# Kernel optimization log

Measured on AMD Instinct MI355X. Metric: run time of the kernel, lower is better.

Reference implementation:

```python
import jax, jax.numpy as jnp
import numpy as np

DEPTH, DIM, HEADS, DIM_HEAD, NBF, MULT = 2, 512, 8, 64, 256, 4
INNER = HEADS * DIM_HEAD


def layernorm(x, g, b, eps=1e-5):
    mu = jnp.mean(x, axis=-1, keepdims=True)
    var = jnp.mean((x - mu) ** 2, axis=-1, keepdims=True)
    return (x - mu) * jax.lax.rsqrt(var + eps) * g + b


def softmax_kernel(data, proj, is_query, eps=1e-4):
    # data: [b,h,n,d], proj: [m,d]  -> phi: [b,h,n,m]  (FAVOR+ positive features)
    d = data.shape[-1]
    normalizer = d ** -0.25
    ratio = proj.shape[0] ** -0.5
    data_dash = jnp.einsum('bhnd,md->bhnm', data * normalizer, proj)
    diag = jnp.sum(data ** 2, axis=-1, keepdims=True) * 0.5 * (normalizer ** 2)
    if is_query:
        m = jnp.max(data_dash, axis=-1, keepdims=True)
    else:
        m = jnp.max(data_dash, axis=(-2, -1), keepdims=True)
    m = jax.lax.stop_gradient(m)
    return ratio * (jnp.exp(data_dash - diag - m) + eps)


def setup_inputs() -> dict:
    key = jax.random.key(0)
    ks = jax.random.split(key, 16)
    s = 0.02
    B, N = 4, 8192
    inp = {
        'x': jax.random.normal(ks[0], (B, N, DIM), jnp.float32),
        'ln1_g': jnp.ones((DEPTH, DIM), jnp.float32),
        'ln1_b': jnp.zeros((DEPTH, DIM), jnp.float32),
        'ln2_g': jnp.ones((DEPTH, DIM), jnp.float32),
        'ln2_b': jnp.zeros((DEPTH, DIM), jnp.float32),
        'Wq': jax.random.normal(ks[1], (DEPTH, DIM, INNER), jnp.float32) * s,
        'bq': jnp.zeros((DEPTH, INNER), jnp.float32),
        'Wk': jax.random.normal(ks[2], (DEPTH, DIM, INNER), jnp.float32) * s,
        'bk': jnp.zeros((DEPTH, INNER), jnp.float32),
        'Wv': jax.random.normal(ks[3], (DEPTH, DIM, INNER), jnp.float32) * s,
        'bv': jnp.zeros((DEPTH, INNER), jnp.float32),
        'Wo': jax.random.normal(ks[4], (DEPTH, INNER, DIM), jnp.float32) * s,
        'bo': jnp.zeros((DEPTH, DIM), jnp.float32),
        'proj': jax.random.normal(ks[5], (DEPTH, NBF, DIM_HEAD), jnp.float32),
        'W1': jax.random.normal(ks[6], (DEPTH, DIM, DIM * MULT), jnp.float32) * s,
        'b1': jnp.zeros((DEPTH, DIM * MULT), jnp.float32),
        'W2': jax.random.normal(ks[7], (DEPTH, DIM * MULT, DIM), jnp.float32) * s,
        'b2': jnp.zeros((DEPTH, DIM), jnp.float32),
    }
    return inp


def reference(x, ln1_g, ln1_b, ln2_g, ln2_b, Wq, bq, Wk, bk, Wv, bv, Wo, bo, proj, W1, b1, W2, b2):
    B, N, D = x.shape
    for i in range(DEPTH):
        # --- PreLayerNorm + FAVOR+ self-attention, residual ---
        y = layernorm(x, ln1_g[i], ln1_b[i])
        q = (y @ Wq[i] + bq[i]).reshape(B, N, HEADS, DIM_HEAD).transpose(0, 2, 1, 3)
        k = (y @ Wk[i] + bk[i]).reshape(B, N, HEADS, DIM_HEAD).transpose(0, 2, 1, 3)
        v = (y @ Wv[i] + bv[i]).reshape(B, N, HEADS, DIM_HEAD).transpose(0, 2, 1, 3)
        qp = softmax_kernel(q, proj[i], True)   # [b,h,n,m]
        kp = softmax_kernel(k, proj[i], False)  # [b,h,n,m]
        # non-causal linear attention: O(n*m*d) instead of O(n^2)
        k_sum = kp.sum(axis=2)                               # [b,h,m]
        d_inv = 1.0 / jnp.einsum('bhnm,bhm->bhn', qp, k_sum)
        ctx = jnp.einsum('bhnm,bhnd->bhmd', kp, v)           # [b,h,m,d]
        o = jnp.einsum('bhmd,bhnm,bhn->bhnd', ctx, qp, d_inv)
        o = o.transpose(0, 2, 1, 3).reshape(B, N, INNER)
        x = x + o @ Wo[i] + bo[i]
        # --- PreLayerNorm + FeedForward (GELU), residual ---
        y = layernorm(x, ln2_g[i], ln2_b[i])
        h = jax.nn.gelu(y @ W1[i] + b1[i], approximate=False)
        x = x + h @ W2[i] + b2[i]
    return x
```

## Files before the change

kernel.cpp:

```cpp
#include <hip/hip_runtime.h>
#include <math.h>

#define DIMX 512
#define HEADS 8
#define DHEAD 64
#define NBFX 256
#define FFD 2048
#define NBX 4
#define SEQ 8192
#define TOK (NBX*SEQ)
#define NBH (NBX*HEADS)
#define VROWS 80
#define NCHUNK 16
#define BK 64

typedef unsigned short u16;
typedef __attribute__((ext_vector_type(8))) short short8;
typedef __attribute__((ext_vector_type(4))) float f32x4;

__device__ __forceinline__ float bf2f(u16 x){ return __uint_as_float(((unsigned)x)<<16); }
__device__ __forceinline__ u16 f2bf(float f){
  unsigned u=__float_as_uint(f);
  return (u16)((u + 0x7FFFu + ((u>>16)&1u))>>16);
}
__device__ __forceinline__ void gload16(const void* g, void* l){
  __builtin_amdgcn_global_load_lds((const __attribute__((address_space(1))) void*)g,
                                   (__attribute__((address_space(3))) void*)l, 16, 0, 0);
}
__device__ __forceinline__ float gelu_f(float v){
  float x=v*0.70710678118654752f;
  float ax=fabsf(x);
  float t=1.0f/(1.0f+0.3275911f*ax);
  float p=t*(0.254829592f+t*(-0.284496736f+t*(1.421413741f+t*(-1.453152027f+t*1.061405429f))));
  float erfv=1.0f-p*__expf(-ax*ax);
  erfv=(x<0.0f)? -erfv : erfv;
  return 0.5f*v*(1.0f+erfv);
}

#define FENCE asm volatile(""::: "memory")
#define BAR() do{ FENCE; __builtin_amdgcn_s_barrier(); FENCE; }while(0)

__global__ void copy_f32(const float4* __restrict__ s, float4* __restrict__ d, int n4){
  int i=blockIdx.x*blockDim.x+threadIdx.x;
  if(i<n4) d[i]=s[i];
}
__global__ void conv_proj(const float* __restrict__ p, u16* __restrict__ o, int n){
  int i=blockIdx.x*blockDim.x+threadIdx.x;
  if(i<n) o[i]=f2bf(p[i]*0.35355339059327373f);
}
__global__ void convT(const float* __restrict__ src, u16* __restrict__ dst, int K, int Ncol){
  __shared__ float t[32][33];
  int k0=blockIdx.y*32, n0=blockIdx.x*32;
  int tx=threadIdx.x, ty=threadIdx.y;
  for(int i=ty;i<32;i+=8) t[i][tx]=src[(size_t)(k0+i)*Ncol + n0+tx];
  __syncthreads();
  for(int i=ty;i<32;i+=8) dst[(size_t)(n0+i)*K + k0+tx]=f2bf(t[tx][i]);
}
__global__ void fill_vt(u16* __restrict__ vt){
  int i=blockIdx.x*blockDim.x+threadIdx.x;
  int n=i&(SEQ-1); int r=(i>>13)&15; int bh=i>>17;
  vt[((size_t)bh*VROWS + 64 + r)*SEQ + n] = (r==0)? (u16)0x3F80 : (u16)0;
}
__global__ void pack_bias(const float* __restrict__ bq, const float* __restrict__ bk,
                          const float* __restrict__ bv, float* __restrict__ o){
  int i=blockIdx.x*blockDim.x+threadIdx.x;
  int l=i/1536, c=i-l*1536;
  const float* s=(c<512)? bq : ((c<1024)? bk : bv);
  o[i]=s[l*512 + (c&511)];
}

__global__ __launch_bounds__(256) void ln_k(const float* __restrict__ x, const float* __restrict__ g,
                                            const float* __restrict__ b, u16* __restrict__ y){
  const int row=blockIdx.x*4 + (threadIdx.x>>6);
  const int ln=threadIdx.x&63;
  const float* xr=x+(size_t)row*DIMX;
  float4 v0=*(const float4*)&xr[ln*8];
  float4 v1=*(const float4*)&xr[ln*8+4];
  float v[8]={v0.x,v0.y,v0.z,v0.w,v1.x,v1.y,v1.z,v1.w};
  float s=0;
  #pragma unroll
  for(int e=0;e<8;e++) s+=v[e];
  #pragma unroll
  for(int m=1;m<64;m<<=1) s+=__shfl_xor(s,m);
  const float mean=s*(1.0f/DIMX);
  float s2=0;
  #pragma unroll
  for(int e=0;e<8;e++){ v[e]-=mean; s2+=v[e]*v[e]; }
  #pragma unroll
  for(int m=1;m<64;m<<=1) s2+=__shfl_xor(s2,m);
  const float rs=rsqrtf(s2*(1.0f/DIMX)+1e-5f);
  u16* yr=y+(size_t)row*DIMX+ln*8;
  u16 pk[8];
  #pragma unroll
  for(int e=0;e<8;e++) pk[e]=f2bf(v[e]*rs*g[ln*8+e]+b[ln*8+e]);
  uint4 pv;
  pv.x=(unsigned)pk[0]|((unsigned)pk[1]<<16); pv.y=(unsigned)pk[2]|((unsigned)pk[3]<<16);
  pv.z=(unsigned)pk[4]|((unsigned)pk[5]<<16); pv.w=(unsigned)pk[6]|((unsigned)pk[7]<<16);
  *(uint4*)yr=pv;
}

#define MFMA16(MH,BF,NH) do{                                                             \
  __builtin_amdgcn_s_setprio(1);                                                         \
  _Pragma("unroll") for(int kk_=0;kk_<2;kk_++)                                           \
    _Pragma("unroll") for(int i_=0;i_<4;i_++)                                            \
      _Pragma("unroll") for(int j_=0;j_<2;j_++)                                          \
        acc[MH][i_][NH][j_]=__builtin_amdgcn_mfma_f32_16x16x32_bf16(af[i_][kk_],BF[j_][kk_],acc[MH][i_][NH][j_],0,0,0); \
  __builtin_amdgcn_s_setprio(0);                                                         \
}while(0)

#define STG(T,HALF,ISB,BUF) do{ if((T)<nt){                                              \
  gload16(gp[ISB][HALF][0]+(size_t)(T)*BK, &lds[BUF][ISB][(HALF)*128 +    wv*8][0]);     \
  gload16(gp[ISB][HALF][1]+(size_t)(T)*BK, &lds[BUF][ISB][(HALF)*128 + 64+wv*8][0]); } }while(0)

#define LDA(BUF,MH) do{                                                                  \
  _Pragma("unroll") for(int i_=0;i_<4;i_++)                                              \
    _Pragma("unroll") for(int kk_=0;kk_<2;kk_++)                                         \
      af[i_][kk_]=*(const short8*)((const u16*)lds[BUF][0] + aoffs[MH][i_][kk_]); }while(0)

#define LDB(BF,BUF,NH) do{                                                               \
  _Pragma("unroll") for(int j_=0;j_<2;j_++)                                              \
    _Pragma("unroll") for(int kk_=0;kk_<2;kk_++)                                         \
      BF[j_][kk_]=*(const short8*)((const u16*)lds[BUF][1] + boffs[NH][j_][kk_]); }while(0)

#define TILE(T,BUF,OBUF) do{                                                             \
  LDB(bf0,BUF,0); LDA(BUF,0);                                                            \
  STG((T)+1,1,0,OBUF);                                                                   \
  BAR(); MFMA16(0,bf0,0); BAR();                                                         \
  LDB(bf1,BUF,1);                                                                        \
  STG((T)+1,1,1,OBUF);                                                                   \
  BAR(); MFMA16(0,bf1,1); BAR();                                                         \
  LDA(BUF,1);                                                                            \
  STG((T)+2,0,1,BUF);                                                                    \
  BAR(); MFMA16(1,bf0,0); BAR();                                                         \
  STG((T)+2,0,0,BUF);                                                                    \
  BAR(); MFMA16(1,bf1,1);                                                                \
  if((T)+2<nt) asm volatile("s_waitcnt vmcnt(4)":::"memory");                            \
  else         asm volatile("s_waitcnt vmcnt(0)":::"memory");                            \
  BAR();                                                                                 \
}while(0)

template<int EPI,int K>
__global__ __launch_bounds__(512,2) void gemm256(const u16* __restrict__ A, const u16* __restrict__ Bt,
                                                 const float* __restrict__ bias, void* __restrict__ outp,
                                                 u16* __restrict__ out2, int Ncol){
  constexpr int nt=K/BK;
  __shared__ u16 lds[2][2][256][64];
  const int tid=threadIdx.x, wv=tid>>6, ln=tid&63;
  const int wr=wv>>2, wc=wv&3;
  const int gx=gridDim.x, gy=gridDim.y;
  const int P=blockIdx.y*gx+blockIdx.x;
  const int band=gy>>3;
  const int xcd=P&7, sI=P>>3;
  const int by=xcd*band + (sI - (sI/band)*band);
  const int bx=sI/band;
  const int m0=by*256, n0=bx*256;
  f32x4 acc[2][4][2][2]={};

  const u16* gp[2][2][2];
  #pragma unroll
  for(int isB=0;isB<2;isB++)
    #pragma unroll
    for(int half=0;half<2;half++)
      #pragma unroll
      for(int s=0;s<2;s++){
        int G=s*512+wv*64+ln;
        int arow=half*128+(G>>3), g=G&7;
        const u16* src=isB? Bt:A;
        int b0=isB? n0:m0;
        gp[isB][half][s]=src+(size_t)(b0+arow)*K+((g^(arow&7))<<3);
      }
  int aoffs[2][4][2], boffs[2][2][2];
  #pragma unroll
  for(int mh=0;mh<2;mh++)
    #pragma unroll
    for(int i=0;i<4;i++){
      int row=wr*128+mh*64+i*16+(ln&15);
      #pragma unroll
      for(int kk=0;kk<2;kk++)
        aoffs[mh][i][kk]=row*64+((((kk*4+(ln>>4)))^(row&7))<<3);
    }
  #pragma unroll
  for(int nh=0;nh<2;nh++)
    #pragma unroll
    for(int j=0;j<2;j++){
      int row=wc*64+nh*32+j*16+(ln&15);
      #pragma unroll
      for(int kk=0;kk<2;kk++)
        boffs[nh][j][kk]=row*64+((((kk*4+(ln>>4)))^(row&7))<<3);
    }

  short8 af[4][2], bf0[2][2], bf1[2][2];

  STG(0,0,0,0); STG(0,1,0,0); STG(0,0,1,0); STG(0,1,1,0);
  STG(1,0,1,1); STG(1,0,0,1);
  asm volatile("s_waitcnt vmcnt(4)":::"memory");
  BAR();

  #pragma unroll 1
  for(int t=0;t<nt;t+=2){
    TILE(t,0,1);
    TILE(t+1,1,0);
  }

  #pragma unroll
  for(int mh=0;mh<2;mh++)
  #pragma unroll
  for(int i=0;i<4;i++)
  #pragma unroll
  for(int nh=0;nh<2;nh++)
  #pragma unroll
  for(int j=0;j<2;j++){
    const int row=m0+wr*128+mh*64+i*16+(ln>>4)*4;
    const int col=n0+wc*64+nh*32+j*16+(ln&15);
    const float bv=bias[col];
    const f32x4 a=acc[mh][i][nh][j];
    if constexpr(EPI==0){
      if(col<1024){
        u16* o=(u16*)outp + (size_t)(col>>9)*TOK*DIMX + (col&511);
        #pragma unroll
        for(int r=0;r<4;r++) o[(size_t)(row+r)*DIMX]=f2bf(a[r]+bv);
      } else {
        const int hd=col-1024, h_=hd>>6, d_=hd&63, b_=row>>13, nn=row&(SEQ-1);
        u16 pk[4];
        #pragma unroll
        for(int r=0;r<4;r++) pk[r]=f2bf(a[r]+bv);
        uint2 pv; pv.x=(unsigned)pk[0]|((unsigned)pk[1]<<16); pv.y=(unsigned)pk[2]|((unsigned)pk[3]<<16);
        *(uint2*)&out2[((size_t)(b_*HEADS+h_)*VROWS+d_)*SEQ+nn]=pv;
      }
    } else if constexpr(EPI==1){
      float* o=(float*)outp;
      #pragma unroll
      for(int r=0;r<4;r++){ size_t ix=(size_t)(row+r)*Ncol+col; o[ix]+=a[r]+bv; }
    } else {
      u16* o=(u16*)outp;
      #pragma unroll
      for(int r=0;r<4;r++)
        o[(size_t)(row+r)*Ncol+col]=f2bf(gelu_f(a[r]+bv));
    }
  }
}

__global__ __launch_bounds__(256) void vsum_k(const u16* __restrict__ vt, float* __restrict__ vs){
  const int gw=blockIdx.x*4 + (threadIdx.x>>6);
  const int ln=threadIdx.x&63;
  const int bh=gw/65, d=gw-bh*65;
  const u16* row=vt+((size_t)bh*VROWS+d)*SEQ;
  float s=0;
  for(int it=0;it<16;it++){
    short8 v=*(const short8*)&row[it*512+ln*8];
    #pragma unroll
    for(int e=0;e<8;e++) s+=bf2f((u16)v[e]);
  }
  #pragma unroll
  for(int m=1;m<64;m<<=1) s+=__shfl_xor(s,m);
  if(ln==0) vs[bh*80+d]=s;
}

__global__ __launch_bounds__(256) void kctx(const u16* __restrict__ kb, const u16* __restrict__ pj,
                                            const u16* __restrict__ vt,
                                            float* __restrict__ part, float* __restrict__ maxb){
  __shared__ u16 kl[64*64];
  __shared__ u16 vl[80*64];
  __shared__ u16 kp_l[128*64];
  __shared__ float dgl[64];
  const int kc=blockIdx.x, half=blockIdx.y, bh=blockIdx.z, b_=bh>>3, h_=bh&7;
  const int tid=threadIdx.x, wv=tid>>6, ln=tid&63;
  short8 pjf[2][2];
  #pragma unroll
  for(int i=0;i<2;i++)
    #pragma unroll
    for(int t=0;t<2;t++)
      pjf[i][t]=*(const short8*)&pj[(size_t)(half*128+wv*32+i*16+(ln&15))*DHEAD + t*32 + (ln>>4)*8];
  f32x4 ctx[2][5]={};
  float m_run=-3.0e38f;
  const u16* vbh=vt+(size_t)bh*VROWS*SEQ;
  for(int s=0;s<8;s++){
    const int n0s=kc*512+s*64;
    const u16* kg=kb+((size_t)(b_*SEQ+n0s))*DIMX + h_*DHEAD;
    #pragma unroll
    for(int cc=0;cc<2;cc++){
      int c=cc*256+wv*64+ln; int t=c>>3, g=c&7;
      gload16(kg+(size_t)t*DIMX+((g^(t&7))*8), &kl[(size_t)(cc*256+wv*64)*8]);
    }
    #pragma unroll
    for(int cc=0;cc<2;cc++){
      int c=cc*256+wv*64+ln; int d=c>>3, g=c&7;
      gload16(vbh+(size_t)d*SEQ+n0s+((g^(d&7))*8), &vl[(size_t)(cc*256+wv*64)*8]);
    }
    if(wv<2){
      int c=512+wv*64+ln; int d=c>>3, g=c&7;
      gload16(vbh+(size_t)d*SEQ+n0s+((g^(d&7))*8), &vl[(size_t)(512+wv*64)*8]);
    }
    __syncthreads();
    if(tid<64){
      float ss=0;
      #pragma unroll
      for(int gg=0;gg<8;gg++){
        short8 kv=*(const short8*)&kl[tid*64 + ((gg+tid)&7)*8];
        #pragma unroll
        for(int e=0;e<8;e++){ float x=bf2f((u16)kv[e]); ss+=x*x; }
      }
      dgl[tid]=ss*0.0625f;
    }
    __syncthreads();
    f32x4 dd[2][4]={};
    #pragma unroll
    for(int tk=0;tk<2;tk++)
      #pragma unroll
      for(int j=0;j<4;j++){
        short8 bk_=*(const short8*)&kl[(j*16+(ln&15))*64 + (((tk*4+(ln>>4))^(ln&7))<<3)];
        #pragma unroll
        for(int i=0;i<2;i++)
          dd[i][j]=__builtin_amdgcn_mfma_f32_16x16x32_bf16(pjf[i][tk],bk_,dd[i][j],0,0,0);
      }
    float mt=-3.0e38f;
    #pragma unroll
    for(int i=0;i<2;i++)
      #pragma unroll
      for(int j=0;j<4;j++)
        #pragma unroll
        for(int r=0;r<4;r++) mt=fmaxf(mt,dd[i][j][r]);
    #pragma unroll
    for(int m=1;m<64;m<<=1) mt=fmaxf(mt,__shfl_xor(mt,m));
    if(mt>m_run){
      float sc=__expf(m_run-mt);
      #pragma unroll
      for(int i=0;i<2;i++)
        #pragma unroll
        for(int j2=0;j2<5;j2++) ctx[i][j2]*=sc;
      m_run=mt;
    }
    #pragma unroll
    for(int j=0;j<4;j++){
      const float dgn=dgl[j*16+(ln&15)];
      #pragma unroll
      for(int i=0;i<2;i++)
        #pragma unroll
        for(int r=0;r<4;r++){
          int m_l=wv*32+i*16+(ln>>4)*4+r;
          float E=__expf(dd[i][j][r]-dgn-m_run);
          kp_l[m_l*64 + (((j*2+((ln>>3)&1))^(m_l&7))<<3) + (ln&7)]=f2bf(E);
        }
    }
    #pragma unroll
    for(int tk=0;tk<2;tk++){
      short8 af2[2];
      #pragma unroll
      for(int i=0;i<2;i++)
        af2[i]=*(const short8*)&kp_l[(wv*32+i*16+(ln&15))*64 + (((tk*4+(ln>>4))^(ln&7))<<3)];
      #pragma unroll
      for(int j2=0;j2<5;j2++){
        short8 bf2=*(const short8*)&vl[(j2*16+(ln&15))*64 + (((tk*4+(ln>>4))^(ln&7))<<3)];
        #pragma unroll
        for(int i=0;i<2;i++)
          ctx[i][j2]=__builtin_amdgcn_mfma_f32_16x16x32_bf16(af2[i],bf2,ctx[i][j2],0,0,0);
      }
    }
    __syncthreads();
  }
  float* po=part + ((size_t)(bh*NCHUNK+kc))*(256*80) + (size_t)half*128*80;
  #pragma unroll
  for(int i=0;i<2;i++)
    #pragma unroll
    for(int j2=0;j2<5;j2++)
      #pragma unroll
      for(int r=0;r<4;r++)
        po[(size_t)(wv*32+i*16+(ln>>4)*4+r)*80 + j2*16+(ln&15)]=ctx[i][j2][r];
  if(ln==0) maxb[bh*128 + kc*8 + half*4 + wv]=m_run;
}

__global__ __launch_bounds__(256) void ctx_reduce(const float* __restrict__ part, const float* __restrict__ maxb,
                                                  const float* __restrict__ vs,
                                                  u16* __restrict__ ctxT, float* __restrict__ ksum){
  __shared__ float mx_s[128];
  __shared__ float sc_s[NCHUNK];
  const int mseg=blockIdx.x, bh=blockIdx.y, tid=threadIdx.x;
  if(tid<128) mx_s[tid]=maxb[(size_t)bh*128+tid];
  __syncthreads();
  float km=-3.0e38f;
  for(int i=0;i<128;i++) km=fmaxf(km,mx_s[i]);
  const int m0=mseg*32;
  const int half=m0>>7, wvv=(m0&127)>>5;
  if(tid<NCHUNK) sc_s[tid]=__expf(mx_s[tid*8+half*4+wvv]-km);
  __syncthreads();
  for(int rep=0;rep<10;rep++){
    int idx=rep*256+tid;
    int mo=idx/80, d=idx-mo*80;
    int m=m0+mo;
    float s=0;
    #pragma unroll
    for(int c=0;c<NCHUNK;c++)
      s+=sc_s[c]*part[((size_t)(bh*NCHUNK+c))*(256*80) + (size_t)m*80 + d];
    float vsd=(d<=64)? vs[bh*80+d] : 0.0f;
    float val=0.0625f*(s + 1e-4f*vsd);
    if(d<64)       ctxT[((size_t)bh*64+d)*NBFX + m]=f2bf(val);
    else if(d==64) ksum[bh*NBFX+m]=val;
  }
}

__global__ void csum_k(const u16* __restrict__ ctxT, const float* __restrict__ ksum, float* __restrict__ cs){
  const int bh=blockIdx.x, t=threadIdx.x;
  if(t<64){
    const u16* r=ctxT+((size_t)bh*64+t)*NBFX;
    float s=0;
    for(int m=0;m<NBFX;m+=8){
      short8 v=*(const short8*)&r[m];
      #pragma unroll
      for(int e=0;e<8;e++) s+=bf2f((u16)v[e]);
    }
    cs[bh*80+t]=s;
  } else if(t==64){
    float s=0;
    for(int m=0;m<NBFX;m++) s+=ksum[bh*NBFX+m];
    cs[bh*80+64]=s;
  }
}

__global__ __launch_bounds__(256) void q_fused(const u16* __restrict__ qb, const u16* __restrict__ pj,
                                               const u16* __restrict__ ctxT, const float* __restrict__ ksum,
                                               const float* __restrict__ cs, u16* __restrict__ ob){
  __shared__ u16 ql[64*64];
  __shared__ u16 qpl[64*136];
  __shared__ float dgs[64];
  __shared__ float mred[4*64], dred[4*64];
  __shared__ float ff_s[64], dinv_s[64];
  const int bh=blockIdx.y, b_=bh>>3, h_=bh&7;
  const int n0=blockIdx.x*64;
  const int tid=threadIdx.x, wv=tid>>6, ln=tid&63;
  const u16* qg=qb+((size_t)(b_*SEQ+n0))*DIMX + h_*DHEAD;
  #pragma unroll
  for(int cc=0;cc<2;cc++){
    int c=cc*256+wv*64+ln; int t=c>>3, g=c&7;
    gload16(qg+(size_t)t*DIMX+((g^(t&7))*8), &ql[(size_t)(cc*256+wv*64)*8]);
  }
  short8 pjf[2][2][2];
  float ks[2][2][4];
  #pragma unroll
  for(int h=0;h<2;h++)
    #pragma unroll
    for(int i=0;i<2;i++){
      #pragma unroll
      for(int t=0;t<2;t++)
        pjf[h][i][t]=*(const short8*)&pj[(size_t)(h*128+wv*32+i*16+(ln&15))*DHEAD + t*32 + (ln>>4)*8];
      #pragma unroll
      for(int r=0;r<4;r++)
        ks[h][i][r]=ksum[bh*NBFX + h*128+wv*32+i*16+(ln>>4)*4+r];
    }
  const float KS=cs[bh*80+64];
  __syncthreads();
  if(tid<64){
    float ss=0;
    #pragma unroll
    for(int gg=0;gg<8;gg++){
      short8 kv=*(const short8*)&ql[tid*64 + ((gg+tid)&7)*8];
      #pragma unroll
      for(int e=0;e<8;e++){ float x=bf2f((u16)kv[e]); ss+=x*x; }
    }
    dgs[tid]=ss*0.0625f;
  }
  __syncthreads();
  float mxp[4]={-3.0e38f,-3.0e38f,-3.0e38f,-3.0e38f};
  float dnp[4]={0,0,0,0};
  f32x4 oc[4]={};
  const u16* cb=ctxT+(size_t)bh*64*NBFX;
  #pragma unroll
  for(int h=0;h<2;h++){
    #pragma unroll
    for(int j=0;j<4;j++){
      f32x4 dq[2]={};
      #pragma unroll
      for(int tk=0;tk<2;tk++){
        short8 bq=*(const short8*)&ql[(j*16+(ln&15))*64 + (((tk*4+(ln>>4))^(ln&7))<<3)];
        #pragma unroll
        for(int i=0;i<2;i++)
          dq[i]=__builtin_amdgcn_mfma_f32_16x16x32_bf16(pjf[h][i][tk],bq,dq[i],0,0,0);
      }
      const float dgn=dgs[j*16+(ln&15)];
      #pragma unroll
      for(int i=0;i<2;i++)
        #pragma unroll
        for(int r=0;r<4;r++){
          float d_=dq[i][r];
          mxp[j]=fmaxf(mxp[j],d_);
          float E=__expf(d_-dgn);
          dnp[j]+=E*ks[h][i][r];
          qpl[(j*16+(ln&15))*136 + wv*32+i*16+(ln>>4)*4+r]=f2bf(E);
        }
    }
    __syncthreads();
    #pragma unroll
    for(int mk2=0;mk2<4;mk2++){
      short8 aq=*(const short8*)&cb[(size_t)(wv*16+(ln&15))*NBFX + h*128 + mk2*32 + (ln>>4)*8];
      #pragma unroll
      for(int j2=0;j2<4;j2++){
        short8 bqp=*(const short8*)&qpl[(j2*16+(ln&15))*136 + mk2*32 + (ln>>4)*8];
        oc[j2]=__builtin_amdgcn_mfma_f32_16x16x32_bf16(aq,bqp,oc[j2],0,0,0);
      }
    }
    __syncthreads();
  }
  #pragma unroll
  for(int j=0;j<4;j++){
    #pragma unroll
    for(int msk=16;msk<64;msk<<=1){
      mxp[j]=fmaxf(mxp[j],__shfl_xor(mxp[j],msk));
      dnp[j]+=__shfl_xor(dnp[j],msk);
    }
  }
  if(ln<16){
    #pragma unroll
    for(int j=0;j<4;j++){ mred[wv*64+j*16+ln]=mxp[j]; dred[wv*64+j*16+ln]=dnp[j]; }
  }
  __syncthreads();
  if(tid<64){
    float mx=fmaxf(fmaxf(mred[tid],mred[64+tid]),fmaxf(mred[128+tid],mred[192+tid]));
    float dn=dred[tid]+dred[64+tid]+dred[128+tid]+dred[192+tid];
    float f=1e-4f*__expf(mx);
    ff_s[tid]=f;
    dinv_s[tid]=1.0f/(dn + f*KS);
  }
  __syncthreads();
  float csr[4];
  #pragma unroll
  for(int r=0;r<4;r++) csr[r]=cs[bh*80 + wv*16+(ln>>4)*4+r];
  u16* og=ob+((size_t)(b_*SEQ+n0))*DIMX + h_*DHEAD;
  #pragma unroll
  for(int j2=0;j2<4;j2++){
    int n=j2*16+(ln&15);
    float f=ff_s[n], di=dinv_s[n];
    u16 pk[4];
    #pragma unroll
    for(int r=0;r<4;r++) pk[r]=f2bf((oc[j2][r]+f*csr[r])*di);
    uint2 pv; pv.x=(unsigned)pk[0]|((unsigned)pk[1]<<16); pv.y=(unsigned)pk[2]|((unsigned)pk[3]<<16);
    *(uint2*)&og[(size_t)n*DIMX + wv*16+(ln>>4)*4]=pv;
  }
}

static constexpr size_t SZ_ACT=(size_t)TOK*DIMX*2;
static constexpr size_t O_Y=0, O_Q=SZ_ACT, O_K=2*SZ_ACT;
static constexpr size_t O_VT=3*SZ_ACT;
static constexpr size_t SZ_VT=(size_t)NBH*VROWS*SEQ*2;
static constexpr size_t O_PART=O_VT+SZ_VT;
static constexpr size_t SZ_PART=(size_t)NBH*NCHUNK*256*80*4;
static constexpr size_t O_CTXT=O_PART+SZ_PART;
static constexpr size_t SZ_CTXT=(size_t)NBH*64*NBFX*2;
static constexpr size_t O_KSUM=O_CTXT+SZ_CTXT;
static constexpr size_t SZ_KSUM=(size_t)NBH*NBFX*4;
static constexpr size_t O_MAX=O_KSUM+SZ_KSUM;
static constexpr size_t SZ_MAX=(size_t)NBH*128*4;
static constexpr size_t O_VSUM=O_MAX+SZ_MAX;
static constexpr size_t SZ_VSUM=(size_t)NBH*80*4;
static constexpr size_t O_CS=O_VSUM+SZ_VSUM;
static constexpr size_t SZ_CS=(size_t)NBH*80*4;
static constexpr size_t O_WQKV=O_CS+SZ_CS;
static constexpr size_t SZ_WQKV=(size_t)2*1536*DIMX*2;
static constexpr size_t O_WOT=O_WQKV+SZ_WQKV;
static constexpr size_t SZ_W=(size_t)2*DIMX*DIMX*2;
static constexpr size_t O_W1T=O_WOT+SZ_W;
static constexpr size_t SZ_W1=(size_t)2*FFD*DIMX*2;
static constexpr size_t O_W2T=O_W1T+SZ_W1;
static constexpr size_t O_PJ=O_W2T+SZ_W1;
static constexpr size_t O_QKVB=O_PJ+(size_t)2*NBFX*DHEAD*2;
static constexpr size_t WS_END=O_QKVB+(size_t)2*1536*4;

extern "C" void kernel_launch(void* const* d_in, const int* in_sizes, int n_in,
                              void* d_out, int out_size, void* d_ws, size_t ws_size,
                              hipStream_t stream){
  (void)in_sizes;(void)n_in;(void)out_size;
  const float* xin =(const float*)d_in[0];
  const float* ln1g=(const float*)d_in[1];
  const float* ln1b=(const float*)d_in[2];
  const float* ln2g=(const float*)d_in[3];
  const float* ln2b=(const float*)d_in[4];
  const float* Wq=(const float*)d_in[5];
  const float* bq=(const float*)d_in[6];
  const float* Wk=(const float*)d_in[7];
  const float* bk=(const float*)d_in[8];
  const float* Wv=(const float*)d_in[9];
  const float* bv=(const float*)d_in[10];
  const float* Wo=(const float*)d_in[11];
  const float* bo=(const float*)d_in[12];
  const float* proj=(const float*)d_in[13];
  const float* W1=(const float*)d_in[14];
  const float* b1=(const float*)d_in[15];
  const float* W2=(const float*)d_in[16];
  const float* b2=(const float*)d_in[17];
  float* xout=(float*)d_out;

  copy_f32<<<(TOK*DIMX/4)/256,256,0,stream>>>((const float4*)xin,(float4*)xout, TOK*DIMX/4);
  if(ws_size < WS_END) return;

  char* ws=(char*)d_ws;
  u16* ybuf =(u16*)(ws+O_Y);
  u16* qbuf =(u16*)(ws+O_Q);
  u16* kbuf =(u16*)(ws+O_K);
  u16* vtb  =(u16*)(ws+O_VT);
  float* partb=(float*)(ws+O_PART);
  u16* ctxtb=(u16*)(ws+O_CTXT);
  float* ksumb=(float*)(ws+O_KSUM);
  float* maxb=(float*)(ws+O_MAX);
  float* vsumb=(float*)(ws+O_VSUM);
  float* csb=(float*)(ws+O_CS);
  u16* wqkvt=(u16*)(ws+O_WQKV);
  u16* wot=(u16*)(ws+O_WOT);
  u16* w1t=(u16*)(ws+O_W1T); u16* w2t=(u16*)(ws+O_W2T);
  u16* pjb=(u16*)(ws+O_PJ);
  float* qkvb=(float*)(ws+O_QKVB);
  u16* hbuf=(u16*)(ws+O_Q);

  for(int l=0;l<2;l++){
    size_t wo=(size_t)l*DIMX*DIMX;
    convT<<<dim3(16,16),dim3(32,8),0,stream>>>(Wq+wo, wqkvt+(size_t)(l*1536+   0)*DIMX, DIMX, DIMX);
    convT<<<dim3(16,16),dim3(32,8),0,stream>>>(Wk+wo, wqkvt+(size_t)(l*1536+ 512)*DIMX, DIMX, DIMX);
    convT<<<dim3(16,16),dim3(32,8),0,stream>>>(Wv+wo, wqkvt+(size_t)(l*1536+1024)*DIMX, DIMX, DIMX);
    convT<<<dim3(16,16),dim3(32,8),0,stream>>>(Wo+wo, wot+wo, DIMX, DIMX);
    size_t w1o=(size_t)l*DIMX*FFD;
    convT<<<dim3(64,16),dim3(32,8),0,stream>>>(W1+w1o, w1t+w1o, DIMX, FFD);
    convT<<<dim3(16,64),dim3(32,8),0,stream>>>(W2+w1o, w2t+w1o, FFD, DIMX);
  }
  conv_proj<<<(2*NBFX*DHEAD)/256,256,0,stream>>>(proj, pjb, 2*NBFX*DHEAD);
  pack_bias<<<12,256,0,stream>>>(bq,bk,bv,qkvb);

  for(int l=0;l<2;l++){
    const u16* wqkvt_l=wqkvt+(size_t)l*1536*DIMX;
    const u16* wot_l=wot+(size_t)l*DIMX*DIMX;
    const u16* w1t_l=w1t+(size_t)l*DIMX*FFD;
    const u16* w2t_l=w2t+(size_t)l*DIMX*FFD;
    const u16* pj_l =pjb+(size_t)l*NBFX*DHEAD;
    const float* qkvb_l=qkvb+(size_t)l*1536;

    ln_k<<<TOK/4,256,0,stream>>>(xout, ln1g+l*DIMX, ln1b+l*DIMX, ybuf);
    fill_vt<<<(NBH*16*SEQ)/256,256,0,stream>>>(vtb);
    gemm256<0,512><<<dim3(6,128),512,0,stream>>>(ybuf, wqkvt_l, qkvb_l, qbuf, vtb, 1536);
    vsum_k<<<520,256,0,stream>>>(vtb, vsumb);
    kctx<<<dim3(NCHUNK,2,32),256,0,stream>>>(kbuf, pj_l, vtb, partb, maxb);
    ctx_reduce<<<dim3(8,32),256,0,stream>>>(partb, maxb, vsumb, ctxtb, ksumb);
    csum_k<<<32,256,0,stream>>>(ctxtb, ksumb, csb);
    q_fused<<<dim3(128,32),256,0,stream>>>(qbuf, pj_l, ctxtb, ksumb, csb, ybuf);
    gemm256<1,512><<<dim3(2,128),512,0,stream>>>(ybuf, wot_l, bo+l*DIMX, xout, nullptr, DIMX);
    ln_k<<<TOK/4,256,0,stream>>>(xout, ln2g+l*DIMX, ln2b+l*DIMX, ybuf);
    gemm256<2,512><<<dim3(8,128),512,0,stream>>>(ybuf, w1t_l, b1+l*FFD, hbuf, nullptr, FFD);
    gemm256<1,2048><<<dim3(2,128),512,0,stream>>>(hbuf, w2t_l, b2+l*DIMX, xout, nullptr, DIMX);
  }
}
```

Before: 1.049 ms.

## Keep residual stream in bf16, regroup GEMM tile swizzle, halve kctx chunks

The fp32 residual stream becomes a bf16 workspace buffer. The input is converted once at the start and expanded back to fp32 at the end, so the layernorm reads and the residual read-modify-write epilogues move half the bytes. The GEMM block-to-tile mapping is regrouped into XCD-aware groups of H row-bands to improve L2 reuse. The kctx sequence chunks are doubled in length, so there are half as many partial contexts to reduce. The cost is that the residual is accumulated in bf16 across four additions, which loses precision.

```diff
diff --git a/kernel.cpp b/kernel.cpp
--- a/kernel.cpp
+++ b/kernel.cpp
@@ -11,7 +11,7 @@
 #define TOK (NBX*SEQ)
 #define NBH (NBX*HEADS)
 #define VROWS 80
-#define NCHUNK 16
+#define NCHUNK 8
 #define BK 64
 
 typedef unsigned short u16;
@@ -44,6 +44,24 @@
   int i=blockIdx.x*blockDim.x+threadIdx.x;
   if(i<n4) d[i]=s[i];
 }
+__global__ void conv_x(const float* __restrict__ x, u16* __restrict__ t){
+  int i=blockIdx.x*blockDim.x+threadIdx.x;
+  const float* xr=x+(size_t)i*8;
+  float4 a=*(const float4*)xr, b=*(const float4*)(xr+4);
+  u16 pk[8]={f2bf(a.x),f2bf(a.y),f2bf(a.z),f2bf(a.w),f2bf(b.x),f2bf(b.y),f2bf(b.z),f2bf(b.w)};
+  uint4 pv;
+  pv.x=(unsigned)pk[0]|((unsigned)pk[1]<<16); pv.y=(unsigned)pk[2]|((unsigned)pk[3]<<16);
+  pv.z=(unsigned)pk[4]|((unsigned)pk[5]<<16); pv.w=(unsigned)pk[6]|((unsigned)pk[7]<<16);
+  *(uint4*)(t+(size_t)i*8)=pv;
+}
+__global__ void expand_k(const u16* __restrict__ t, float* __restrict__ o){
+  int i=blockIdx.x*blockDim.x+threadIdx.x;
+  short8 v=*(const short8*)(t+(size_t)i*8);
+  float* orr=o+(size_t)i*8;
+  float4 f0={bf2f((u16)v[0]),bf2f((u16)v[1]),bf2f((u16)v[2]),bf2f((u16)v[3])};
+  float4 f1={bf2f((u16)v[4]),bf2f((u16)v[5]),bf2f((u16)v[6]),bf2f((u16)v[7])};
+  *(float4*)orr=f0; *(float4*)(orr+4)=f1;
+}
 __global__ void conv_proj(const float* __restrict__ p, u16* __restrict__ o, int n){
   int i=blockIdx.x*blockDim.x+threadIdx.x;
   if(i<n) o[i]=f2bf(p[i]*0.35355339059327373f);
@@ -69,14 +87,15 @@
   o[i]=s[l*512 + (c&511)];
 }
 
-__global__ __launch_bounds__(256) void ln_k(const float* __restrict__ x, const float* __restrict__ g,
+__global__ __launch_bounds__(256) void ln_k(const u16* __restrict__ x, const float* __restrict__ g,
                                             const float* __restrict__ b, u16* __restrict__ y){
   const int row=blockIdx.x*4 + (threadIdx.x>>6);
   const int ln=threadIdx.x&63;
-  const float* xr=x+(size_t)row*DIMX;
-  float4 v0=*(const float4*)&xr[ln*8];
-  float4 v1=*(const float4*)&xr[ln*8+4];
-  float v[8]={v0.x,v0.y,v0.z,v0.w,v1.x,v1.y,v1.z,v1.w};
+  const u16* xr=x+(size_t)row*DIMX;
+  short8 xv=*(const short8*)(xr+ln*8);
+  float v[8];
+  #pragma unroll
+  for(int e=0;e<8;e++) v[e]=bf2f((u16)xv[e]);
   float s=0;
   #pragma unroll
   for(int e=0;e<8;e++) s+=v[e];
@@ -144,15 +163,18 @@
                                                  const float* __restrict__ bias, void* __restrict__ outp,
                                                  u16* __restrict__ out2, int Ncol){
   constexpr int nt=K/BK;
+  constexpr int HS=(K==2048)?1:2;
+  constexpr int H=1<<HS;
   __shared__ u16 lds[2][2][256][64];
   const int tid=threadIdx.x, wv=tid>>6, ln=tid&63;
   const int wr=wv>>2, wc=wv&3;
-  const int gx=gridDim.x, gy=gridDim.y;
+  const int gx=gridDim.x;
   const int P=blockIdx.y*gx+blockIdx.x;
-  const int band=gy>>3;
-  const int xcd=P&7, sI=P>>3;
-  const int by=xcd*band + (sI - (sI/band)*band);
-  const int bx=sI/band;
+  const int grp=8*H*gx;
+  const int G=P/grp, R=P-G*grp;
+  const int xcd=R&7, s=R>>3;
+  const int by=(G*8+xcd)*H + (s&(H-1));
+  const int bx=s>>HS;
   const int m0=by*256, n0=bx*256;
   f32x4 acc[2][4][2][2]={};
 
@@ -162,12 +184,12 @@
     #pragma unroll
     for(int half=0;half<2;half++)
       #pragma unroll
-      for(int s=0;s<2;s++){
-        int G=s*512+wv*64+ln;
-        int arow=half*128+(G>>3), g=G&7;
+      for(int ss=0;ss<2;ss++){
+        int Gg=ss*512+wv*64+ln;
+        int arow=half*128+(Gg>>3), g=Gg&7;
         const u16* src=isB? Bt:A;
         int b0=isB? n0:m0;
-        gp[isB][half][s]=src+(size_t)(b0+arow)*K+((g^(arow&7))<<3);
+        gp[isB][half][ss]=src+(size_t)(b0+arow)*K+((g^(arow&7))<<3);
       }
   int aoffs[2][4][2], boffs[2][2][2];
   #pragma unroll
@@ -228,9 +250,12 @@
         *(uint2*)&out2[((size_t)(b_*HEADS+h_)*VROWS+d_)*SEQ+nn]=pv;
       }
     } else if constexpr(EPI==1){
-      float* o=(float*)outp;
-      #pragma unroll
-      for(int r=0;r<4;r++){ size_t ix=(size_t)(row+r)*Ncol+col; o[ix]+=a[r]+bv; }
+      u16* o=(u16*)outp;
+      #pragma unroll
+      for(int r=0;r<4;r++){
+        size_t ix=(size_t)(row+r)*Ncol+col;
+        o[ix]=f2bf(bf2f(o[ix])+a[r]+bv);
+      }
     } else {
       u16* o=(u16*)outp;
       #pragma unroll
@@ -274,8 +299,8 @@
   f32x4 ctx[2][5]={};
   float m_run=-3.0e38f;
   const u16* vbh=vt+(size_t)bh*VROWS*SEQ;
-  for(int s=0;s<8;s++){
-    const int n0s=kc*512+s*64;
+  for(int s=0;s<16;s++){
+    const int n0s=kc*1024+s*64;
     const u16* kg=kb+((size_t)(b_*SEQ+n0s))*DIMX + h_*DHEAD;
     #pragma unroll
     for(int cc=0;cc<2;cc++){
@@ -366,19 +391,19 @@
       #pragma unroll
       for(int r=0;r<4;r++)
         po[(size_t)(wv*32+i*16+(ln>>4)*4+r)*80 + j2*16+(ln&15)]=ctx[i][j2][r];
-  if(ln==0) maxb[bh*128 + kc*8 + half*4 + wv]=m_run;
+  if(ln==0) maxb[bh*64 + kc*8 + half*4 + wv]=m_run;
 }
 
 __global__ __launch_bounds__(256) void ctx_reduce(const float* __restrict__ part, const float* __restrict__ maxb,
                                                   const float* __restrict__ vs,
                                                   u16* __restrict__ ctxT, float* __restrict__ ksum){
-  __shared__ float mx_s[128];
+  __shared__ float mx_s[64];
   __shared__ float sc_s[NCHUNK];
   const int mseg=blockIdx.x, bh=blockIdx.y, tid=threadIdx.x;
-  if(tid<128) mx_s[tid]=maxb[(size_t)bh*128+tid];
+  if(tid<64) mx_s[tid]=maxb[(size_t)bh*64+tid];
   __syncthreads();
   float km=-3.0e38f;
-  for(int i=0;i<128;i++) km=fmaxf(km,mx_s[i]);
+  for(int i=0;i<64;i++) km=fmaxf(km,mx_s[i]);
   const int m0=mseg*32;
   const int half=m0>>7, wvv=(m0&127)>>5;
   if(tid<NCHUNK) sc_s[tid]=__expf(mx_s[tid*8+half*4+wvv]-km);
@@ -537,8 +562,9 @@
 }
 
 static constexpr size_t SZ_ACT=(size_t)TOK*DIMX*2;
-static constexpr size_t O_Y=0, O_Q=SZ_ACT, O_K=2*SZ_ACT;
-static constexpr size_t O_VT=3*SZ_ACT;
+static constexpr size_t O_X=0;
+static constexpr size_t O_Y=SZ_ACT, O_Q=2*SZ_ACT, O_K=3*SZ_ACT;
+static constexpr size_t O_VT=4*SZ_ACT;
 static constexpr size_t SZ_VT=(size_t)NBH*VROWS*SEQ*2;
 static constexpr size_t O_PART=O_VT+SZ_VT;
 static constexpr size_t SZ_PART=(size_t)NBH*NCHUNK*256*80*4;
@@ -547,12 +573,13 @@
 static constexpr size_t O_KSUM=O_CTXT+SZ_CTXT;
 static constexpr size_t SZ_KSUM=(size_t)NBH*NBFX*4;
 static constexpr size_t O_MAX=O_KSUM+SZ_KSUM;
-static constexpr size_t SZ_MAX=(size_t)NBH*128*4;
+static constexpr size_t SZ_MAX=(size_t)NBH*64*4;
 static constexpr size_t O_VSUM=O_MAX+SZ_MAX;
 static constexpr size_t SZ_VSUM=(size_t)NBH*80*4;
 static constexpr size_t O_CS=O_VSUM+SZ_VSUM;
 static constexpr size_t SZ_CS=(size_t)NBH*80*4;
-static constexpr size_t O_WQKV=O_CS+SZ_CS;
+static constexpr size_t O_WQKV=(size_t)192*1024*1024;
+static_assert(O_CS+SZ_CS <= O_WQKV, "small buffers must end below weight region");
 static constexpr size_t SZ_WQKV=(size_t)2*1536*DIMX*2;
 static constexpr size_t O_WOT=O_WQKV+SZ_WQKV;
 static constexpr size_t SZ_W=(size_t)2*DIMX*DIMX*2;
@@ -587,10 +614,13 @@
   const float* b2=(const float*)d_in[17];
   float* xout=(float*)d_out;
 
-  copy_f32<<<(TOK*DIMX/4)/256,256,0,stream>>>((const float4*)xin,(float4*)xout, TOK*DIMX/4);
-  if(ws_size < WS_END) return;
+  if(ws_size < WS_END){
+    copy_f32<<<(TOK*DIMX/4)/256,256,0,stream>>>((const float4*)xin,(float4*)xout, TOK*DIMX/4);
+    return;
+  }
 
   char* ws=(char*)d_ws;
+  u16* xtr  =(u16*)(ws+O_X);
   u16* ybuf =(u16*)(ws+O_Y);
   u16* qbuf =(u16*)(ws+O_Q);
   u16* kbuf =(u16*)(ws+O_K);
@@ -620,6 +650,7 @@
   }
   conv_proj<<<(2*NBFX*DHEAD)/256,256,0,stream>>>(proj, pjb, 2*NBFX*DHEAD);
   pack_bias<<<12,256,0,stream>>>(bq,bk,bv,qkvb);
+  conv_x<<<(TOK*DIMX/8)/256,256,0,stream>>>(xin, xtr);
 
   for(int l=0;l<2;l++){
     const u16* wqkvt_l=wqkvt+(size_t)l*1536*DIMX;
@@ -629,7 +660,7 @@
     const u16* pj_l =pjb+(size_t)l*NBFX*DHEAD;
     const float* qkvb_l=qkvb+(size_t)l*1536;
 
-    ln_k<<<TOK/4,256,0,stream>>>(xout, ln1g+l*DIMX, ln1b+l*DIMX, ybuf);
+    ln_k<<<TOK/4,256,0,stream>>>(xtr, ln1g+l*DIMX, ln1b+l*DIMX, ybuf);
     fill_vt<<<(NBH*16*SEQ)/256,256,0,stream>>>(vtb);
     gemm256<0,512><<<dim3(6,128),512,0,stream>>>(ybuf, wqkvt_l, qkvb_l, qbuf, vtb, 1536);
     vsum_k<<<520,256,0,stream>>>(vtb, vsumb);
@@ -637,9 +668,10 @@
     ctx_reduce<<<dim3(8,32),256,0,stream>>>(partb, maxb, vsumb, ctxtb, ksumb);
     csum_k<<<32,256,0,stream>>>(ctxtb, ksumb, csb);
     q_fused<<<dim3(128,32),256,0,stream>>>(qbuf, pj_l, ctxtb, ksumb, csb, ybuf);
-    gemm256<1,512><<<dim3(2,128),512,0,stream>>>(ybuf, wot_l, bo+l*DIMX, xout, nullptr, DIMX);
-    ln_k<<<TOK/4,256,0,stream>>>(xout, ln2g+l*DIMX, ln2b+l*DIMX, ybuf);
+    gemm256<1,512><<<dim3(2,128),512,0,stream>>>(ybuf, wot_l, bo+l*DIMX, xtr, nullptr, DIMX);
+    ln_k<<<TOK/4,256,0,stream>>>(xtr, ln2g+l*DIMX, ln2b+l*DIMX, ybuf);
     gemm256<2,512><<<dim3(8,128),512,0,stream>>>(ybuf, w1t_l, b1+l*FFD, hbuf, nullptr, FFD);
-    gemm256<1,2048><<<dim3(2,128),512,0,stream>>>(hbuf, w2t_l, b2+l*DIMX, xout, nullptr, DIMX);
-  }
-}
+    gemm256<1,2048><<<dim3(2,128),512,0,stream>>>(hbuf, w2t_l, b2+l*DIMX, xtr, nullptr, DIMX);
+  }
+  expand_k<<<(TOK*DIMX/8)/256,256,0,stream>>>(xtr, xout);
+}
```

Result: faster. 1.004 ms (-4.4%).
